# Performance work log

Measured on AMD Instinct MI355X. Metric: run time of the kernel, lower is better.

## Reference

```python
import jax, jax.numpy as jnp
import numpy as np

B, T, D, A = 16, 2048, 512, 64


def setup_inputs() -> dict:
    key = jax.random.key(0)
    ks = jax.random.split(key, 7)
    s = 1.0 / np.sqrt(D)
    return {
        "inp": jax.random.normal(ks[0], (B, T, D), dtype=jnp.float32),
        "Wq": jax.random.normal(ks[1], (D, A), dtype=jnp.float32) * s,
        "bq": jax.random.normal(ks[2], (A,), dtype=jnp.float32) * 0.01,
        "Wk": jax.random.normal(ks[3], (D, A), dtype=jnp.float32) * s,
        "bk": jax.random.normal(ks[4], (A,), dtype=jnp.float32) * 0.01,
        "Wv": jax.random.normal(ks[5], (D, A), dtype=jnp.float32) * s,
        "bv": jax.random.normal(ks[6], (A,), dtype=jnp.float32) * 0.01,
    }


def reference(inp, Wq, bq, Wk, bk, Wv, bv):
    # Projections: (B,T,D) @ (D,A) -> (B,T,A)
    Q = inp @ Wq + bq
    K = inp @ Wk + bk
    V = inp @ Wv + bv
    # Scaled QK^T: (B,T,T)
    scores = jnp.einsum("btd,bsd->bts", Q, K) / jnp.sqrt(jnp.float32(A))
    # Sign-based K padding mask: mask[b, s] = sign(|sum_a K[b,s,a]|)
    k_mask = jnp.sign(jnp.abs(K.sum(axis=-1)))  # (B,T)
    scores = jnp.where(k_mask[:, None, :] == 0, jnp.float32(1e-8), scores)
    att = jax.nn.softmax(scores, axis=-1)
    # Sign-based Q mask broadcast along the key axis (faithful to Mask module)
    q_mask = jnp.sign(jnp.abs(Q.sum(axis=-1)))  # (B,T)
    att = att * q_mask[:, None, :]
    # dropout_keep_prob == 1 -> dropout is identity
    ctx = jnp.einsum("bts,bsa->bta", att, V)  # (B,T,A)
    # inp^T @ ctx -> (B,D,A), then sum over A -> (B,D)
    out = jnp.einsum("btd,bta->bd", inp, ctx)
    return out
```

## Files before the change

### kernel.cpp

```cpp
#include <hip/hip_runtime.h>

#define B_ 16
#define T_ 2048
#define D_ 512
#define A_ 64

typedef __bf16 bf16x8 __attribute__((ext_vector_type(8)));
typedef float  f32x4  __attribute__((ext_vector_type(4)));

__device__ inline unsigned short f2bf(float f){
    union { float f; unsigned u; } x; x.f = f;
    unsigned r = x.u + 0x7fffu + ((x.u >> 16) & 1u);
    return (unsigned short)(r >> 16);
}

__device__ inline bf16x8 ldfrag(const unsigned short* p){
    uint4 v = *reinterpret_cast<const uint4*>(p);
    return __builtin_bit_cast(bf16x8, v);
}

__global__ void setup_kernel(const float* __restrict__ Wq, const float* __restrict__ Wk,
                             const float* __restrict__ Wv, unsigned short* __restrict__ WcT,
                             float* __restrict__ out){
    int e = blockIdx.x * 256 + threadIdx.x;
    int j = e >> 9;
    int d = e & 511;
    float v;
    if (j < 64)       v = Wq[d * 64 + j];
    else if (j < 128) v = Wk[d * 64 + (j - 64)];
    else              v = Wv[d * 64 + (j - 128)];
    WcT[j * 512 + d] = f2bf(v);
    if (e < B_ * D_) out[e] = 0.f;
}

__global__ __launch_bounds__(256) void proj_kernel(
    const float* __restrict__ inp, const unsigned short* __restrict__ WcT,
    const float* __restrict__ bq, const float* __restrict__ bk, const float* __restrict__ bv,
    unsigned short* __restrict__ Qb, unsigned short* __restrict__ Kb,
    float* __restrict__ wv, float* __restrict__ kf)
{
    __shared__ __align__(16) unsigned short As[128 * 40];
    __shared__ __align__(16) unsigned short Bs[192 * 40];
    const int tid  = threadIdx.x;
    const int r0   = blockIdx.x * 128;
    const int lane = tid & 63, wvid = tid >> 6;
    const int m = lane & 15, q = lane >> 4;

    f32x4 acc[12][2];
    #pragma unroll
    for (int t = 0; t < 12; t++){
        acc[t][0] = (f32x4){0.f,0.f,0.f,0.f};
        acc[t][1] = (f32x4){0.f,0.f,0.f,0.f};
    }

    for (int kk = 0; kk < 512; kk += 32){
        #pragma unroll
        for (int i = 0; i < 4; i++){
            int row = i * 32 + (tid >> 3);
            int col = (tid & 7) * 4;
            float4 v = *reinterpret_cast<const float4*>(&inp[(size_t)(r0 + row) * 512 + kk + col]);
            ushort4 h; h.x = f2bf(v.x); h.y = f2bf(v.y); h.z = f2bf(v.z); h.w = f2bf(v.w);
            *reinterpret_cast<ushort4*>(&As[row * 40 + col]) = h;
        }
        #pragma unroll
        for (int it = 0; it < 3; it++){
            int sidx = it * 256 + tid;
            int row = sidx >> 2, seg = sidx & 3;
            uint4 v = *reinterpret_cast<const uint4*>(&WcT[row * 512 + kk + seg * 8]);
            *reinterpret_cast<uint4*>(&Bs[row * 40 + seg * 8]) = v;
        }
        __syncthreads();
        bf16x8 a0 = ldfrag(&As[(32 * wvid + m)      * 40 + q * 8]);
        bf16x8 a1 = ldfrag(&As[(32 * wvid + 16 + m) * 40 + q * 8]);
        #pragma unroll
        for (int t = 0; t < 12; t++){
            bf16x8 bfr = ldfrag(&Bs[(t * 16 + m) * 40 + q * 8]);
            acc[t][0] = __builtin_amdgcn_mfma_f32_16x16x32_bf16(a0, bfr, acc[t][0], 0, 0, 0);
            acc[t][1] = __builtin_amdgcn_mfma_f32_16x16x32_bf16(a1, bfr, acc[t][1], 0, 0, 0);
        }
        __syncthreads();
    }

    float bqv[4], bkv[4], bvv[4];
    #pragma unroll
    for (int t = 0; t < 4; t++){
        bqv[t] = bq[t * 16 + m]; bkv[t] = bk[t * 16 + m]; bvv[t] = bv[t * 16 + m];
    }
    #pragma unroll
    for (int f = 0; f < 2; f++){
        float qs[4], ks[4], vs[4];
        #pragma unroll
        for (int i = 0; i < 4; i++){
            size_t r = (size_t)r0 + 32 * wvid + 16 * f + q * 4 + i;
            float sq = 0.f, sk = 0.f, sv = 0.f;
            #pragma unroll
            for (int t = 0; t < 4; t++){
                float vq = acc[t][f][i]     + bqv[t];
                float vk = acc[t + 4][f][i] + bkv[t];
                float vvv = acc[t + 8][f][i] + bvv[t];
                Qb[r * 64 + t * 16 + m] = f2bf(vq);
                Kb[r * 64 + t * 16 + m] = f2bf(vk);
                sq += vq; sk += vk; sv += vvv;
            }
            qs[i] = sq; ks[i] = sk; vs[i] = sv;
        }
        #pragma unroll
        for (int s = 1; s < 16; s <<= 1){
            #pragma unroll
            for (int i = 0; i < 4; i++){
                qs[i] += __shfl_xor(qs[i], s);
                ks[i] += __shfl_xor(ks[i], s);
                vs[i] += __shfl_xor(vs[i], s);
            }
        }
        if (m == 0){
            #pragma unroll
            for (int i = 0; i < 4; i++){
                size_t r = (size_t)r0 + 32 * wvid + 16 * f + q * 4 + i;
                float qmask = (qs[i] == 0.f) ? 0.f : 1.f;
                wv[r] = qmask * vs[i];
                kf[r] = (ks[i] == 0.f) ? 1.f : 0.f;
            }
        }
    }
}

__global__ __launch_bounds__(256) void attn_kernel(
    const unsigned short* __restrict__ Qb, const unsigned short* __restrict__ Kb,
    const float* __restrict__ wv, const float* __restrict__ kf, float* __restrict__ c)
{
    __shared__ __align__(16) unsigned short Qs[64 * 72];
    __shared__ __align__(16) unsigned short Ks[64 * 72];
    __shared__ float wsh[64];
    __shared__ float kfs[64];
    const int tid = threadIdx.x;
    const int b   = blockIdx.y;
    const int t0  = blockIdx.x * 64;
    const int lane = tid & 63, wvid = tid >> 6;
    const int m = lane & 15, q = lane >> 4;
    const size_t base = (size_t)b * T_;

    {
        int row = tid >> 2, seg = tid & 3;
        const uint4* src = reinterpret_cast<const uint4*>(&Qb[(base + t0 + row) * 64 + seg * 16]);
        uint4* dst = reinterpret_cast<uint4*>(&Qs[row * 72 + seg * 16]);
        dst[0] = src[0]; dst[1] = src[1];
    }

    float mrun[4], num[4], den[4];
    #pragma unroll
    for (int i = 0; i < 4; i++){ mrun[i] = -1e30f; num[i] = 0.f; den[i] = 0.f; }

    for (int s0 = 0; s0 < T_; s0 += 64){
        __syncthreads();
        {
            int row = tid >> 2, seg = tid & 3;
            const uint4* src = reinterpret_cast<const uint4*>(&Kb[(base + s0 + row) * 64 + seg * 16]);
            uint4* dst = reinterpret_cast<uint4*>(&Ks[row * 72 + seg * 16]);
            dst[0] = src[0]; dst[1] = src[1];
            if (tid < 64)       wsh[tid]      = wv[base + s0 + tid];
            else if (tid < 128) kfs[tid - 64] = kf[base + s0 + tid - 64];
        }
        __syncthreads();
        bf16x8 a0 = ldfrag(&Qs[(16 * wvid + m) * 72 + q * 8]);
        bf16x8 a1 = ldfrag(&Qs[(16 * wvid + m) * 72 + 32 + q * 8]);
        f32x4 sacc[4];
        #pragma unroll
        for (int st = 0; st < 4; st++){
            bf16x8 b0 = ldfrag(&Ks[(st * 16 + m) * 72 + q * 8]);
            bf16x8 b1 = ldfrag(&Ks[(st * 16 + m) * 72 + 32 + q * 8]);
            f32x4 z = (f32x4){0.f,0.f,0.f,0.f};
            z = __builtin_amdgcn_mfma_f32_16x16x32_bf16(a0, b0, z, 0, 0, 0);
            z = __builtin_amdgcn_mfma_f32_16x16x32_bf16(a1, b1, z, 0, 0, 0);
            sacc[st] = z;
        }
        float wcol[4], kcol[4];
        #pragma unroll
        for (int st = 0; st < 4; st++){ wcol[st] = wsh[st * 16 + m]; kcol[st] = kfs[st * 16 + m]; }
        float sc[4][4];
        #pragma unroll
        for (int st = 0; st < 4; st++)
            #pragma unroll
            for (int i = 0; i < 4; i++)
                sc[st][i] = (kcol[st] != 0.f) ? 1e-8f : sacc[st][i] * 0.125f;
        #pragma unroll
        for (int i = 0; i < 4; i++){
            float rm = fmaxf(fmaxf(sc[0][i], sc[1][i]), fmaxf(sc[2][i], sc[3][i]));
            #pragma unroll
            for (int s = 1; s < 16; s <<= 1) rm = fmaxf(rm, __shfl_xor(rm, s));
            float nm  = fmaxf(mrun[i], rm);
            float fac = __expf(mrun[i] - nm);
            num[i] *= fac; den[i] *= fac; mrun[i] = nm;
            #pragma unroll
            for (int st = 0; st < 4; st++){
                float e = __expf(sc[st][i] - nm);
                den[i] += e; num[i] += e * wcol[st];
            }
        }
    }
    #pragma unroll
    for (int s = 1; s < 16; s <<= 1){
        #pragma unroll
        for (int i = 0; i < 4; i++){ num[i] += __shfl_xor(num[i], s); den[i] += __shfl_xor(den[i], s); }
    }
    if (m == 0){
        #pragma unroll
        for (int i = 0; i < 4; i++)
            c[base + t0 + 16 * wvid + q * 4 + i] = num[i] / den[i];
    }
}

__global__ __launch_bounds__(256) void out_kernel(
    const float* __restrict__ inp, const float* __restrict__ c, float* __restrict__ out)
{
    const int tid = threadIdx.x;
    const int b   = blockIdx.y;
    const int t0  = blockIdx.x * 64;
    const size_t base = (size_t)b * T_;
    float a0 = 0.f, a1 = 0.f;
    for (int t = 0; t < 64; t++){
        float ct = c[base + t0 + t];
        const float* row = inp + (base + t0 + t) * 512;
        a0 += row[tid] * ct;
        a1 += row[tid + 256] * ct;
    }
    atomicAdd(&out[b * 512 + tid], a0);
    atomicAdd(&out[b * 512 + tid + 256], a1);
}

extern "C" void kernel_launch(void* const* d_in, const int* in_sizes, int n_in,
                              void* d_out, int out_size, void* d_ws, size_t ws_size,
                              hipStream_t stream)
{
    const float* inp = (const float*)d_in[0];
    const float* Wq  = (const float*)d_in[1];
    const float* bq  = (const float*)d_in[2];
    const float* Wk  = (const float*)d_in[3];
    const float* bk  = (const float*)d_in[4];
    const float* Wv  = (const float*)d_in[5];
    const float* bv  = (const float*)d_in[6];
    float* out = (float*)d_out;

    char* ws = (char*)d_ws;
    unsigned short* WcT = (unsigned short*)(ws);
    unsigned short* Qb  = (unsigned short*)(ws + 262144);
    unsigned short* Kb  = (unsigned short*)(ws + 262144 + 4194304);
    float* wvp = (float*)(ws + 262144 + 2 * 4194304);
    float* kfp = (float*)(ws + 262144 + 2 * 4194304 + 131072);
    float* cc  = (float*)(ws + 262144 + 2 * 4194304 + 2 * 131072);

    setup_kernel<<<384, 256, 0, stream>>>(Wq, Wk, Wv, WcT, out);
    proj_kernel<<<256, 256, 0, stream>>>(inp, WcT, bq, bk, bv, Qb, Kb, wvp, kfp);
    attn_kernel<<<dim3(32, 16), 256, 0, stream>>>(Qb, Kb, wvp, kfp, cc);
    out_kernel<<<dim3(32, 16), 256, 0, stream>>>(inp, cc, out);
}
```

Baseline: 183.1 us.

## Fold V projection into summed weights, split attention over keys, drop online max

```diff
diff --git a/kernel.cpp b/kernel.cpp
--- a/kernel.cpp
+++ b/kernel.cpp
@@ -3,7 +3,6 @@
 #define B_ 16
 #define T_ 2048
 #define D_ 512
-#define A_ 64
 
 typedef __bf16 bf16x8 __attribute__((ext_vector_type(8)));
 typedef float  f32x4  __attribute__((ext_vector_type(4)));
@@ -19,213 +18,194 @@
     return __builtin_bit_cast(bf16x8, v);
 }
 
+
 __global__ void setup_kernel(const float* __restrict__ Wq, const float* __restrict__ Wk,
-                             const float* __restrict__ Wv, unsigned short* __restrict__ WcT,
-                             float* __restrict__ out){
+                             const float* __restrict__ Wv, const float* __restrict__ bq,
+                             const float* __restrict__ bk, const float* __restrict__ bv,
+                             unsigned short* __restrict__ WcT, float* __restrict__ bsum,
+                             float* __restrict__ numden, float* __restrict__ out)
+{
     int e = blockIdx.x * 256 + threadIdx.x;
-    int j = e >> 9;
-    int d = e & 511;
-    float v;
-    if (j < 64)       v = Wq[d * 64 + j];
-    else if (j < 128) v = Wk[d * 64 + (j - 64)];
-    else              v = Wv[d * 64 + (j - 128)];
-    WcT[j * 512 + d] = f2bf(v);
-    if (e < B_ * D_) out[e] = 0.f;
+    if (e < 73728){
+        int j = e >> 9, d = e & 511;
+        float v;
+        if (j < 64)       v = Wq[d * 64 + j];
+        else if (j < 128) v = Wk[d * 64 + (j - 64)];
+        else if (j == 128){ v = 0.f; for (int a = 0; a < 64; a++) v += Wq[d * 64 + a]; }
+        else if (j == 129){ v = 0.f; for (int a = 0; a < 64; a++) v += Wk[d * 64 + a]; }
+        else if (j == 130){ v = 0.f; for (int a = 0; a < 64; a++) v += Wv[d * 64 + a]; }
+        else v = 0.f;
+        WcT[j * 512 + d] = f2bf(v);
+    } else if (e < 73744){
+        int mm = e - 73728;
+        float s = 0.f;
+        if (mm == 0)      for (int a = 0; a < 64; a++) s += bq[a];
+        else if (mm == 1) for (int a = 0; a < 64; a++) s += bk[a];
+        else if (mm == 2) for (int a = 0; a < 64; a++) s += bv[a];
+        bsum[mm] = s;
+    } else if (e < 139280){
+        numden[e - 73744] = 0.f;
+    } else if (e < 147472){
+        out[e - 139280] = 0.f;
+    }
 }
 
 __global__ __launch_bounds__(256) void proj_kernel(
     const float* __restrict__ inp, const unsigned short* __restrict__ WcT,
-    const float* __restrict__ bq, const float* __restrict__ bk, const float* __restrict__ bv,
+    const float* __restrict__ bq, const float* __restrict__ bk,
+    const float* __restrict__ bsum,
     unsigned short* __restrict__ Qb, unsigned short* __restrict__ Kb,
-    float* __restrict__ wv, float* __restrict__ kf)
-{
-    __shared__ __align__(16) unsigned short As[128 * 40];
-    __shared__ __align__(16) unsigned short Bs[192 * 40];
+    float2* __restrict__ wkf)
+{
+    __shared__ __align__(16) unsigned short As[64 * 40];
+    __shared__ __align__(16) unsigned short Bs[144 * 40];
     const int tid  = threadIdx.x;
-    const int r0   = blockIdx.x * 128;
+    const int r0   = blockIdx.x * 64;
     const int lane = tid & 63, wvid = tid >> 6;
     const int m = lane & 15, q = lane >> 4;
 
-    f32x4 acc[12][2];
-    #pragma unroll
-    for (int t = 0; t < 12; t++){
-        acc[t][0] = (f32x4){0.f,0.f,0.f,0.f};
-        acc[t][1] = (f32x4){0.f,0.f,0.f,0.f};
-    }
+    f32x4 acc[9];
+    #pragma unroll
+    for (int t = 0; t < 9; t++) acc[t] = (f32x4){0.f, 0.f, 0.f, 0.f};
+
+    const int arow = tid >> 3;
+    const int acol = (tid & 7) * 4;
 
     for (int kk = 0; kk < 512; kk += 32){
         #pragma unroll
-        for (int i = 0; i < 4; i++){
-            int row = i * 32 + (tid >> 3);
-            int col = (tid & 7) * 4;
-            float4 v = *reinterpret_cast<const float4*>(&inp[(size_t)(r0 + row) * 512 + kk + col]);
+        for (int i = 0; i < 2; i++){
+            int row = i * 32 + arow;
+            float4 v = *reinterpret_cast<const float4*>(&inp[(size_t)(r0 + row) * 512 + kk + acol]);
             ushort4 h; h.x = f2bf(v.x); h.y = f2bf(v.y); h.z = f2bf(v.z); h.w = f2bf(v.w);
-            *reinterpret_cast<ushort4*>(&As[row * 40 + col]) = h;
+            *reinterpret_cast<ushort4*>(&As[row * 40 + acol]) = h;
         }
         #pragma unroll
         for (int it = 0; it < 3; it++){
-            int sidx = it * 256 + tid;
-            int row = sidx >> 2, seg = sidx & 3;
-            uint4 v = *reinterpret_cast<const uint4*>(&WcT[row * 512 + kk + seg * 8]);
-            *reinterpret_cast<uint4*>(&Bs[row * 40 + seg * 8]) = v;
+            int idx = it * 256 + tid;
+            if (idx < 576){
+                int row = idx >> 2, seg = idx & 3;
+                uint4 v = *reinterpret_cast<const uint4*>(&WcT[row * 512 + kk + seg * 8]);
+                *reinterpret_cast<uint4*>(&Bs[row * 40 + seg * 8]) = v;
+            }
         }
         __syncthreads();
-        bf16x8 a0 = ldfrag(&As[(32 * wvid + m)      * 40 + q * 8]);
-        bf16x8 a1 = ldfrag(&As[(32 * wvid + 16 + m) * 40 + q * 8]);
-        #pragma unroll
-        for (int t = 0; t < 12; t++){
+        bf16x8 a = ldfrag(&As[(16 * wvid + m) * 40 + q * 8]);
+        #pragma unroll
+        for (int t = 0; t < 9; t++){
             bf16x8 bfr = ldfrag(&Bs[(t * 16 + m) * 40 + q * 8]);
-            acc[t][0] = __builtin_amdgcn_mfma_f32_16x16x32_bf16(a0, bfr, acc[t][0], 0, 0, 0);
-            acc[t][1] = __builtin_amdgcn_mfma_f32_16x16x32_bf16(a1, bfr, acc[t][1], 0, 0, 0);
+            acc[t] = __builtin_amdgcn_mfma_f32_16x16x32_bf16(a, bfr, acc[t], 0, 0, 0);
         }
         __syncthreads();
     }
 
-    float bqv[4], bkv[4], bvv[4];
-    #pragma unroll
-    for (int t = 0; t < 4; t++){
-        bqv[t] = bq[t * 16 + m]; bkv[t] = bk[t * 16 + m]; bvv[t] = bv[t * 16 + m];
-    }
-    #pragma unroll
-    for (int f = 0; f < 2; f++){
-        float qs[4], ks[4], vs[4];
-        #pragma unroll
-        for (int i = 0; i < 4; i++){
-            size_t r = (size_t)r0 + 32 * wvid + 16 * f + q * 4 + i;
-            float sq = 0.f, sk = 0.f, sv = 0.f;
-            #pragma unroll
-            for (int t = 0; t < 4; t++){
-                float vq = acc[t][f][i]     + bqv[t];
-                float vk = acc[t + 4][f][i] + bkv[t];
-                float vvv = acc[t + 8][f][i] + bvv[t];
-                Qb[r * 64 + t * 16 + m] = f2bf(vq);
-                Kb[r * 64 + t * 16 + m] = f2bf(vk);
-                sq += vq; sk += vk; sv += vvv;
-            }
-            qs[i] = sq; ks[i] = sk; vs[i] = sv;
-        }
-        #pragma unroll
-        for (int s = 1; s < 16; s <<= 1){
+    float bqv[4], bkv[4];
+    #pragma unroll
+    for (int t = 0; t < 4; t++){ bqv[t] = bq[t * 16 + m]; bkv[t] = bk[t * 16 + m]; }
+    const float bs = bsum[m];
+
+    #pragma unroll
+    for (int i = 0; i < 4; i++){
+        size_t r = (size_t)r0 + 16 * wvid + q * 4 + i;
+        #pragma unroll
+        for (int t = 0; t < 4; t++)
+            Qb[r * 64 + t * 16 + m] = f2bf(acc[t][i] + bqv[t]);
+        #pragma unroll
+        for (int t = 0; t < 4; t++)
+            Kb[r * 64 + t * 16 + m] = f2bf(acc[t + 4][i] + bkv[t]);
+        float val = acc[8][i] + bs;
+        float qsv = __shfl(val, (lane & 48));
+        float ksv = __shfl(val, (lane & 48) | 1);
+        float vsv = __shfl(val, (lane & 48) | 2);
+        if (m == 0)
+            wkf[r] = make_float2((qsv == 0.f) ? 0.f : vsv, (ksv == 0.f) ? 1.f : 0.f);
+    }
+}
+
+__global__ __launch_bounds__(256) void attn_kernel(
+    const unsigned short* __restrict__ Qb, const unsigned short* __restrict__ Kb,
+    const float2* __restrict__ wkf, float* __restrict__ num_g, float* __restrict__ den_g)
+{
+    const int tid  = threadIdx.x;
+    const int lane = tid & 63, wvid = tid >> 6;
+    const int m = lane & 15, q = lane >> 4;
+    const int b  = blockIdx.y;
+    const int t0 = blockIdx.x * 64 + wvid * 16;
+    const int s0 = blockIdx.z * 512;
+    const size_t base = (size_t)b * T_;
+
+    const unsigned short* qp = &Qb[(base + t0 + m) * 64 + q * 8];
+    bf16x8 a0 = ldfrag(qp);
+    bf16x8 a1 = ldfrag(qp + 32);
+
+    float num[4] = {0.f, 0.f, 0.f, 0.f}, den[4] = {0.f, 0.f, 0.f, 0.f};
+
+    for (int it = 0; it < 8; it++){
+        int s = s0 + it * 64;
+        const unsigned short* kb = &Kb[(base + s) * 64];
+        f32x4 z[4];
+        float2 wf[4];
+        #pragma unroll
+        for (int st = 0; st < 4; st++){
+            const unsigned short* kp = kb + (st * 16 + m) * 64 + q * 8;
+            bf16x8 b0 = ldfrag(kp);
+            bf16x8 b1 = ldfrag(kp + 32);
+            wf[st] = wkf[base + s + st * 16 + m];
+            f32x4 zz = (f32x4){0.f, 0.f, 0.f, 0.f};
+            zz = __builtin_amdgcn_mfma_f32_16x16x32_bf16(a0, b0, zz, 0, 0, 0);
+            zz = __builtin_amdgcn_mfma_f32_16x16x32_bf16(a1, b1, zz, 0, 0, 0);
+            z[st] = zz;
+        }
+        #pragma unroll
+        for (int st = 0; st < 4; st++){
+            float w = wf[st].x;
+            bool km = (wf[st].y != 0.f);
             #pragma unroll
             for (int i = 0; i < 4; i++){
-                qs[i] += __shfl_xor(qs[i], s);
-                ks[i] += __shfl_xor(ks[i], s);
-                vs[i] += __shfl_xor(vs[i], s);
+                float e = km ? 1.0f : exp2f(z[st][i] * 0.18033688f);
+                den[i] += e;
+                num[i] = fmaf(e, w, num[i]);
             }
         }
-        if (m == 0){
-            #pragma unroll
-            for (int i = 0; i < 4; i++){
-                size_t r = (size_t)r0 + 32 * wvid + 16 * f + q * 4 + i;
-                float qmask = (qs[i] == 0.f) ? 0.f : 1.f;
-                wv[r] = qmask * vs[i];
-                kf[r] = (ks[i] == 0.f) ? 1.f : 0.f;
-            }
-        }
-    }
-}
-
-__global__ __launch_bounds__(256) void attn_kernel(
-    const unsigned short* __restrict__ Qb, const unsigned short* __restrict__ Kb,
-    const float* __restrict__ wv, const float* __restrict__ kf, float* __restrict__ c)
-{
-    __shared__ __align__(16) unsigned short Qs[64 * 72];
-    __shared__ __align__(16) unsigned short Ks[64 * 72];
-    __shared__ float wsh[64];
-    __shared__ float kfs[64];
-    const int tid = threadIdx.x;
-    const int b   = blockIdx.y;
-    const int t0  = blockIdx.x * 64;
-    const int lane = tid & 63, wvid = tid >> 6;
-    const int m = lane & 15, q = lane >> 4;
-    const size_t base = (size_t)b * T_;
-
-    {
-        int row = tid >> 2, seg = tid & 3;
-        const uint4* src = reinterpret_cast<const uint4*>(&Qb[(base + t0 + row) * 64 + seg * 16]);
-        uint4* dst = reinterpret_cast<uint4*>(&Qs[row * 72 + seg * 16]);
-        dst[0] = src[0]; dst[1] = src[1];
-    }
-
-    float mrun[4], num[4], den[4];
-    #pragma unroll
-    for (int i = 0; i < 4; i++){ mrun[i] = -1e30f; num[i] = 0.f; den[i] = 0.f; }
-
-    for (int s0 = 0; s0 < T_; s0 += 64){
-        __syncthreads();
-        {
-            int row = tid >> 2, seg = tid & 3;
-            const uint4* src = reinterpret_cast<const uint4*>(&Kb[(base + s0 + row) * 64 + seg * 16]);
-            uint4* dst = reinterpret_cast<uint4*>(&Ks[row * 72 + seg * 16]);
-            dst[0] = src[0]; dst[1] = src[1];
-            if (tid < 64)       wsh[tid]      = wv[base + s0 + tid];
-            else if (tid < 128) kfs[tid - 64] = kf[base + s0 + tid - 64];
-        }
-        __syncthreads();
-        bf16x8 a0 = ldfrag(&Qs[(16 * wvid + m) * 72 + q * 8]);
-        bf16x8 a1 = ldfrag(&Qs[(16 * wvid + m) * 72 + 32 + q * 8]);
-        f32x4 sacc[4];
-        #pragma unroll
-        for (int st = 0; st < 4; st++){
-            bf16x8 b0 = ldfrag(&Ks[(st * 16 + m) * 72 + q * 8]);
-            bf16x8 b1 = ldfrag(&Ks[(st * 16 + m) * 72 + 32 + q * 8]);
-            f32x4 z = (f32x4){0.f,0.f,0.f,0.f};
-            z = __builtin_amdgcn_mfma_f32_16x16x32_bf16(a0, b0, z, 0, 0, 0);
-            z = __builtin_amdgcn_mfma_f32_16x16x32_bf16(a1, b1, z, 0, 0, 0);
-            sacc[st] = z;
-        }
-        float wcol[4], kcol[4];
-        #pragma unroll
-        for (int st = 0; st < 4; st++){ wcol[st] = wsh[st * 16 + m]; kcol[st] = kfs[st * 16 + m]; }
-        float sc[4][4];
-        #pragma unroll
-        for (int st = 0; st < 4; st++)
-            #pragma unroll
-            for (int i = 0; i < 4; i++)
-                sc[st][i] = (kcol[st] != 0.f) ? 1e-8f : sacc[st][i] * 0.125f;
+    }
+    #pragma unroll
+    for (int s = 1; s < 16; s <<= 1){
         #pragma unroll
         for (int i = 0; i < 4; i++){
-            float rm = fmaxf(fmaxf(sc[0][i], sc[1][i]), fmaxf(sc[2][i], sc[3][i]));
-            #pragma unroll
-            for (int s = 1; s < 16; s <<= 1) rm = fmaxf(rm, __shfl_xor(rm, s));
-            float nm  = fmaxf(mrun[i], rm);
-            float fac = __expf(mrun[i] - nm);
-            num[i] *= fac; den[i] *= fac; mrun[i] = nm;
-            #pragma unroll
-            for (int st = 0; st < 4; st++){
-                float e = __expf(sc[st][i] - nm);
-                den[i] += e; num[i] += e * wcol[st];
-            }
-        }
-    }
-    #pragma unroll
-    for (int s = 1; s < 16; s <<= 1){
-        #pragma unroll
-        for (int i = 0; i < 4; i++){ num[i] += __shfl_xor(num[i], s); den[i] += __shfl_xor(den[i], s); }
+            num[i] += __shfl_xor(num[i], s);
+            den[i] += __shfl_xor(den[i], s);
+        }
     }
     if (m == 0){
         #pragma unroll
-        for (int i = 0; i < 4; i++)
-            c[base + t0 + 16 * wvid + q * 4 + i] = num[i] / den[i];
+        for (int i = 0; i < 4; i++){
+            atomicAdd(&num_g[base + t0 + q * 4 + i], num[i]);
+            atomicAdd(&den_g[base + t0 + q * 4 + i], den[i]);
+        }
     }
 }
 
 __global__ __launch_bounds__(256) void out_kernel(
-    const float* __restrict__ inp, const float* __restrict__ c, float* __restrict__ out)
-{
+    const float* __restrict__ inp, const float* __restrict__ num_g,
+    const float* __restrict__ den_g, float* __restrict__ out)
+{
+    __shared__ float csh[64];
     const int tid = threadIdx.x;
     const int b   = blockIdx.y;
     const int t0  = blockIdx.x * 64;
     const size_t base = (size_t)b * T_;
+    if (tid < 64) csh[tid] = num_g[base + t0 + tid] / den_g[base + t0 + tid];
+    __syncthreads();
+    const float2* ip = reinterpret_cast<const float2*>(inp + (base + t0) * 512);
     float a0 = 0.f, a1 = 0.f;
+    #pragma unroll 4
     for (int t = 0; t < 64; t++){
-        float ct = c[base + t0 + t];
-        const float* row = inp + (base + t0 + t) * 512;
-        a0 += row[tid] * ct;
-        a1 += row[tid + 256] * ct;
-    }
-    atomicAdd(&out[b * 512 + tid], a0);
-    atomicAdd(&out[b * 512 + tid + 256], a1);
+        float ct = csh[t];
+        float2 v = ip[(size_t)t * 256 + tid];
+        a0 = fmaf(v.x, ct, a0);
+        a1 = fmaf(v.y, ct, a1);
+    }
+    atomicAdd(&out[b * 512 + 2 * tid],     a0);
+    atomicAdd(&out[b * 512 + 2 * tid + 1], a1);
 }
 
 extern "C" void kernel_launch(void* const* d_in, const int* in_sizes, int n_in,
@@ -243,14 +223,15 @@
 
     char* ws = (char*)d_ws;
     unsigned short* WcT = (unsigned short*)(ws);
+    float* bsum         = (float*)(ws + 147456);
     unsigned short* Qb  = (unsigned short*)(ws + 262144);
-    unsigned short* Kb  = (unsigned short*)(ws + 262144 + 4194304);
-    float* wvp = (float*)(ws + 262144 + 2 * 4194304);
-    float* kfp = (float*)(ws + 262144 + 2 * 4194304 + 131072);
-    float* cc  = (float*)(ws + 262144 + 2 * 4194304 + 2 * 131072);
-
-    setup_kernel<<<384, 256, 0, stream>>>(Wq, Wk, Wv, WcT, out);
-    proj_kernel<<<256, 256, 0, stream>>>(inp, WcT, bq, bk, bv, Qb, Kb, wvp, kfp);
-    attn_kernel<<<dim3(32, 16), 256, 0, stream>>>(Qb, Kb, wvp, kfp, cc);
-    out_kernel<<<dim3(32, 16), 256, 0, stream>>>(inp, cc, out);
-}
+    unsigned short* Kb  = (unsigned short*)(ws + 4456448);
+    float2* wkf         = (float2*)(ws + 8650752);
+    float* num_g        = (float*)(ws + 8912896);
+    float* den_g        = (float*)(ws + 9043968);
+
+    setup_kernel<<<577, 256, 0, stream>>>(Wq, Wk, Wv, bq, bk, bv, WcT, bsum, num_g, out);
+    proj_kernel<<<512, 256, 0, stream>>>(inp, WcT, bq, bk, bsum, Qb, Kb, wkf);
+    attn_kernel<<<dim3(32, 16, 4), 256, 0, stream>>>(Qb, Kb, wkf, num_g, den_g);
+    out_kernel<<<dim3(32, 16), 256, 0, stream>>>(inp, num_g, den_g, out);
+}
```

After: 210.4 us. +14.9%, slower.
